# Optimization experiments

Measured on AMD Instinct MI355X. Metric: run time of the kernel, lower is better.

## Reference

```python
import jax, jax.numpy as jnp
import numpy as np

HIDDEN = 1024
HEADS = 16
HEAD = HIDDEN // HEADS


def _ternary_weight(key, shape):
    g = jax.random.normal(key, shape, dtype=jnp.float32)
    return jnp.where(jnp.abs(g) < 0.6, 0.0, jnp.sign(g)).astype(jnp.float32)


def setup_inputs() -> dict:
    key = jax.random.key(0)
    ks = jax.random.split(key, 10)
    x = jax.random.normal(ks[0], (2, 2048, HIDDEN), dtype=jnp.float32)
    d = {"x": x}
    names = ["q", "k", "v", "o"]
    for i, n in enumerate(names):
        d[f"w_{n}"] = _ternary_weight(ks[1 + i], (HIDDEN, HIDDEN))
        d[f"s_{n}"] = jnp.float32(0.02)  # per-layer dequant scale
        d[f"b_{n}"] = jax.random.normal(ks[5 + i], (HIDDEN,), dtype=jnp.float32) * 0.02
    return d


def _tlin(x, w, s, b):
    # dequantized ternary linear: x @ (s * w).T + b
    return jnp.einsum("bsh,oh->bso", x, w) * s + b


def reference(x, w_q, s_q, b_q, w_k, s_k, b_k, w_v, s_v, b_v, w_o, s_o, b_o):
    B, S, H = x.shape
    def split_heads(t):
        return t.reshape(B, S, HEADS, HEAD).transpose(0, 2, 1, 3)  # [B, nH, S, hd]
    q = split_heads(_tlin(x, w_q, s_q, b_q))
    k = split_heads(_tlin(x, w_k, s_k, b_k))
    v = split_heads(_tlin(x, w_v, s_v, b_v))
    scores = jnp.einsum("bhqd,bhkd->bhqk", q, k) / jnp.sqrt(jnp.float32(HEAD))
    attn = jax.nn.softmax(scores, axis=-1)
    ctx = jnp.einsum("bhqk,bhkd->bhqd", attn, v)
    ctx = ctx.transpose(0, 2, 1, 3).reshape(B, S, H)
    return _tlin(ctx, w_o, s_o, b_o)
```

## Files before the change

### kernel.cpp

```cpp
#include <hip/hip_runtime.h>
#include <hip/hip_bf16.h>

typedef unsigned short u16;
typedef __bf16 bf16x8 __attribute__((ext_vector_type(8)));
typedef __bf16 bf16x4 __attribute__((ext_vector_type(4)));
typedef float f32x4 __attribute__((ext_vector_type(4)));
typedef unsigned short u16x8 __attribute__((ext_vector_type(8)));

__device__ inline u16 f2bf(float f) {
    union { float f; unsigned u; } v; v.f = f;
    unsigned r = v.u + 0x7fffu + ((v.u >> 16) & 1u);
    return (u16)(r >> 16);
}

__global__ void convert_kernel(const float* __restrict__ x,
                               const float* __restrict__ wq, const float* __restrict__ wk,
                               const float* __restrict__ wv, const float* __restrict__ wo,
                               u16* __restrict__ dst) {
    long g = (long)blockIdx.x * blockDim.x + threadIdx.x;
    const float* src; long base;
    const long GX = 1048576, GW = 262144;
    if (g < GX)            { src = x;  base = 0; }
    else if (g < GX + GW)  { src = wq; base = GX; }
    else if (g < GX + 2*GW){ src = wk; base = GX + GW; }
    else if (g < GX + 3*GW){ src = wv; base = GX + 2*GW; }
    else                   { src = wo; base = GX + 3*GW; }
    long rel = g - base;
    float4 v = reinterpret_cast<const float4*>(src)[rel];
    ushort4 o;
    o.x = f2bf(v.x); o.y = f2bf(v.y); o.z = f2bf(v.z); o.w = f2bf(v.w);
    reinterpret_cast<ushort4*>(dst)[g] = o;
}

__global__ void __launch_bounds__(512)
qkv_gemm(const u16* __restrict__ x_bf,
         const u16* __restrict__ wq, const u16* __restrict__ wk, const u16* __restrict__ wv,
         const float* __restrict__ sq, const float* __restrict__ sk, const float* __restrict__ sv,
         const float* __restrict__ bq, const float* __restrict__ bk, const float* __restrict__ bv,
         u16* __restrict__ q_ws, u16* __restrict__ k_ws, u16* __restrict__ v_ws) {
    __shared__ __align__(16) u16 As[2][128 * 64];
    __shared__ __align__(16) u16 Bs[2][128 * 64];
    const int z = blockIdx.z;
    const u16* W   = (z == 0) ? wq : (z == 1) ? wk : wv;
    const float* sp = (z == 0) ? sq : (z == 1) ? sk : sv;
    const float* bp = (z == 0) ? bq : (z == 1) ? bk : bv;
    u16* dst = (z == 0) ? q_ws : (z == 1) ? k_ws : v_ws;
    const float extra = (z == 0) ? 0.125f * 1.44269504088896f : 1.0f;
    const int t0 = blockIdx.x * 128, n0 = blockIdx.y * 128;

    const int tid = threadIdx.x;
    const int wid = tid >> 6, lane = tid & 63, quad = lane >> 4, ln = lane & 15;
    const int wm = wid >> 2, wn = wid & 3;

    const bool stA = (wid < 4);
    const u16* gbase = stA ? x_bf : W;
    const int r0 = stA ? t0 : n0;
    const int cbase = (wid & 3) * 4;

    f32x4 acc[4][2];
#pragma unroll
    for (int im = 0; im < 4; im++)
#pragma unroll
        for (int in = 0; in < 2; in++) acc[im][in] = (f32x4){0.f, 0.f, 0.f, 0.f};

    const int sb   = cbase * 1024 + lane * 16;
    const int srow = sb >> 7;
    const int scb  = (sb & 127) ^ ((srow & 7) << 4);

#define Q_STAGE(buf, k0)                                                              \
    {                                                                                 \
        const u16* g = gbase + (long)(r0 + srow) * 1024 + (k0) + (scb >> 1);          \
        u16* d = (stA ? &As[buf][0] : &Bs[buf][0]) + cbase * 512;                     \
        _Pragma("unroll")                                                             \
        for (int i = 0; i < 4; i++) {                                                 \
            __builtin_amdgcn_global_load_lds(                                         \
                (const __attribute__((address_space(1))) void*)(g + (long)i * 8 * 1024), \
                (__attribute__((address_space(3))) void*)(d + i * 512), 16, 0, 0);    \
        }                                                                             \
    }

    Q_STAGE(0, 0);
    __syncthreads();

    int cur = 0;
    for (int k0 = 0; k0 < 1024; k0 += 64) {
        if (k0 + 64 < 1024) Q_STAGE(cur ^ 1, k0 + 64);
        const char* Ac = (const char*)&As[cur][0];
        const char* Bc = (const char*)&Bs[cur][0];
#pragma unroll
        for (int ks = 0; ks < 2; ks++) {
            bf16x8 af[4], bfr[2];
#pragma unroll
            for (int im = 0; im < 4; im++) {
                int r = wm * 64 + im * 16 + ln;
                int byt = (r * 128 + ks * 64 + quad * 16) ^ ((r & 7) << 4);
                af[im] = *reinterpret_cast<const bf16x8*>(Ac + byt);
            }
#pragma unroll
            for (int in = 0; in < 2; in++) {
                int r = wn * 32 + in * 16 + ln;
                int byt = (r * 128 + ks * 64 + quad * 16) ^ ((r & 7) << 4);
                bfr[in] = *reinterpret_cast<const bf16x8*>(Bc + byt);
            }
#pragma unroll
            for (int im = 0; im < 4; im++)
#pragma unroll
                for (int in = 0; in < 2; in++)
                    acc[im][in] = __builtin_amdgcn_mfma_f32_16x16x32_bf16(af[im], bfr[in], acc[im][in], 0, 0, 0);
        }
        __syncthreads();
        cur ^= 1;
    }
#undef Q_STAGE

    const float s = sp[0] * extra;
#pragma unroll
    for (int in = 0; in < 2; in++) {
        int col = n0 + wn * 32 + in * 16 + ln;
        float bias = bp[col] * extra;
        int h = col >> 6, d = col & 63;
#pragma unroll
        for (int im = 0; im < 4; im++) {
            int rbase = t0 + wm * 64 + im * 16 + quad * 4;
#pragma unroll
            for (int j2 = 0; j2 < 4; j2++) {
                int t = rbase + j2;
                int b = t >> 11, ss = t & 2047;
                int bh = b * 16 + h;
                float val = acc[im][in][j2] * s + bias;
                long idx = (z < 2) ? ((long)(bh * 2048 + ss) * 64 + d)
                                   : ((long)(bh * 64 + d) * 2048 + ss);
                dst[idx] = f2bf(val);
            }
        }
    }
}

#define LDP 72

__global__ void __launch_bounds__(512)
attn_kernel(const u16* __restrict__ q_ws, const u16* __restrict__ k_ws,
            const u16* __restrict__ v_ws, u16* __restrict__ ctx) {
    __shared__ __align__(16) u16 Kb[2][4096];
    __shared__ __align__(16) u16 Vb[2][4096];
    __shared__ u16 Pt[128 * LDP];

    const int tid = threadIdx.x;
    const int wid = tid >> 6, lane = tid & 63, quad = lane >> 4, ln = lane & 15;

    const int f   = blockIdx.x + 16 * blockIdx.y;
    const int xcd = f & 7, j = f >> 3;
    const int bh  = xcd * 4 + (j >> 4);
    const int q0  = (j & 15) * 128;

    const u16* qbase = q_ws + (long)bh * 2048 * 64;
    const u16* kbase = k_ws + (long)bh * 2048 * 64;
    const u16* vbase = v_ws + (long)bh * 64 * 2048;

    const int srow = wid * 8 + (lane >> 3);
    const int sel  = 8 * ((lane & 7) ^ ((lane >> 3) & 7));
    const int xr = (ln & 7) << 4;

    bf16x8 aq[2];
#pragma unroll
    for (int ks = 0; ks < 2; ks++)
        aq[ks] = *reinterpret_cast<const bf16x8*>(
            qbase + (long)(q0 + wid * 16 + ln) * 64 + ks * 32 + quad * 8);

    bf16x8 vones;
#pragma unroll
    for (int i = 0; i < 8; i++) vones[i] = (__bf16)1.0f;

    f32x4 acc_o[4];
    f32x4 acc_l = (f32x4){0.f, 0.f, 0.f, 0.f};
#pragma unroll
    for (int dt = 0; dt < 4; dt++) acc_o[dt] = (f32x4){0.f, 0.f, 0.f, 0.f};

    const u16* kp = kbase + (long)srow * 64 + sel;
    const u16* vp = vbase + (long)srow * 2048 + sel;

    __builtin_amdgcn_global_load_lds((const __attribute__((address_space(1))) void*)kp,
                                     (__attribute__((address_space(3))) void*)(&Kb[0][wid * 512]),
                                     16, 0, 0);
    __builtin_amdgcn_global_load_lds((const __attribute__((address_space(1))) void*)vp,
                                     (__attribute__((address_space(3))) void*)(&Vb[0][wid * 512]),
                                     16, 0, 0);
    kp += 4096; vp += 64;
    __syncthreads();

    int cur = 0;
    for (int kt = 0; kt < 2048; kt += 64) {
        if (kt + 64 < 2048) {
            __builtin_amdgcn_global_load_lds((const __attribute__((address_space(1))) void*)kp,
                                             (__attribute__((address_space(3))) void*)(&Kb[cur ^ 1][wid * 512]),
                                             16, 0, 0);
            __builtin_amdgcn_global_load_lds((const __attribute__((address_space(1))) void*)vp,
                                             (__attribute__((address_space(3))) void*)(&Vb[cur ^ 1][wid * 512]),
                                             16, 0, 0);
            kp += 4096; vp += 64;
        }
        const char* Kc = (const char*)(&Kb[cur][0]);
        const char* Vc = (const char*)(&Vb[cur][0]);

#pragma unroll
        for (int k8 = 0; k8 < 4; k8++) {
            bf16x8 a0 = *reinterpret_cast<const bf16x8*>(
                Kc + (k8 * 16 + ln) * 128 + ((quad * 16) ^ xr));
            bf16x8 a1 = *reinterpret_cast<const bf16x8*>(
                Kc + (k8 * 16 + ln) * 128 + ((64 + quad * 16) ^ xr));
            f32x4 t = (f32x4){0.f, 0.f, 0.f, 0.f};
            __builtin_amdgcn_s_setprio(1);
            t = __builtin_amdgcn_mfma_f32_16x16x32_bf16(a0, aq[0], t, 0, 0, 0);
            t = __builtin_amdgcn_mfma_f32_16x16x32_bf16(a1, aq[1], t, 0, 0, 0);
            __builtin_amdgcn_s_setprio(0);
            __bf16 p0 = (__bf16)__builtin_amdgcn_exp2f(t[0]);
            __bf16 p1 = (__bf16)__builtin_amdgcn_exp2f(t[1]);
            __bf16 p2 = (__bf16)__builtin_amdgcn_exp2f(t[2]);
            __bf16 p3 = (__bf16)__builtin_amdgcn_exp2f(t[3]);
            *reinterpret_cast<bf16x4*>(Pt + (wid * 16 + ln) * LDP + k8 * 16 + quad * 4)
                = (bf16x4){p0, p1, p2, p3};
        }

#pragma unroll
        for (int step = 0; step < 2; step++) {
            bf16x8 ap = *reinterpret_cast<const bf16x8*>(
                Pt + (wid * 16 + ln) * LDP + step * 32 + quad * 8);
            bf16x8 bv0 = *reinterpret_cast<const bf16x8*>(
                Vc + (0 * 16 + ln) * 128 + ((step * 64 + quad * 16) ^ xr));
            bf16x8 bv1 = *reinterpret_cast<const bf16x8*>(
                Vc + (1 * 16 + ln) * 128 + ((step * 64 + quad * 16) ^ xr));
            bf16x8 bv2 = *reinterpret_cast<const bf16x8*>(
                Vc + (2 * 16 + ln) * 128 + ((step * 64 + quad * 16) ^ xr));
            bf16x8 bv3 = *reinterpret_cast<const bf16x8*>(
                Vc + (3 * 16 + ln) * 128 + ((step * 64 + quad * 16) ^ xr));
            __builtin_amdgcn_s_setprio(1);
            acc_o[0] = __builtin_amdgcn_mfma_f32_16x16x32_bf16(ap, bv0, acc_o[0], 0, 0, 0);
            acc_o[1] = __builtin_amdgcn_mfma_f32_16x16x32_bf16(ap, bv1, acc_o[1], 0, 0, 0);
            acc_o[2] = __builtin_amdgcn_mfma_f32_16x16x32_bf16(ap, bv2, acc_o[2], 0, 0, 0);
            acc_o[3] = __builtin_amdgcn_mfma_f32_16x16x32_bf16(ap, bv3, acc_o[3], 0, 0, 0);
            acc_l    = __builtin_amdgcn_mfma_f32_16x16x32_bf16(ap, vones, acc_l, 0, 0, 0);
            __builtin_amdgcn_s_setprio(0);
        }
        __syncthreads();
        cur ^= 1;
    }

    const int b = bh >> 4, h = bh & 15;
#pragma unroll
    for (int j2 = 0; j2 < 4; j2++) {
        float rinv = 1.0f / acc_l[j2];
        int t = b * 2048 + q0 + wid * 16 + quad * 4 + j2;
#pragma unroll
        for (int dt = 0; dt < 4; dt++) {
            float val = acc_o[dt][j2] * rinv;
            ctx[(long)t * 1024 + h * 64 + dt * 16 + ln] = f2bf(val);
        }
    }
}

__global__ void __launch_bounds__(512)
o_gemm(const u16* __restrict__ ctx, const u16* __restrict__ wo,
       const float* __restrict__ so, const float* __restrict__ bo,
       float* __restrict__ out) {
    __shared__ __align__(16) u16 As[2][128 * 64];
    __shared__ __align__(16) u16 Bs[2][128 * 64];
    const int tid = threadIdx.x;
    const int wid = tid >> 6, lane = tid & 63, quad = lane >> 4, ln = lane & 15;
    const int wm = wid >> 2, wn = wid & 3;
    const int t0 = blockIdx.x * 128, n0 = blockIdx.y * 128;

    const bool stA = (wid < 4);
    const u16* gbase = stA ? ctx : wo;
    const int r0 = stA ? t0 : n0;
    const int cbase = (wid & 3) * 4;

    f32x4 acc[4][2];
#pragma unroll
    for (int im = 0; im < 4; im++)
#pragma unroll
        for (int in = 0; in < 2; in++) acc[im][in] = (f32x4){0.f, 0.f, 0.f, 0.f};

    const int sb   = cbase * 1024 + lane * 16;
    const int srow = sb >> 7;
    const int scb  = (sb & 127) ^ ((srow & 7) << 4);

#define O_STAGE(buf, k0)                                                              \
    {                                                                                 \
        const u16* g = gbase + (long)(r0 + srow) * 1024 + (k0) + (scb >> 1);          \
        u16* d = (stA ? &As[buf][0] : &Bs[buf][0]) + cbase * 512;                     \
        _Pragma("unroll")                                                             \
        for (int i = 0; i < 4; i++) {                                                 \
            __builtin_amdgcn_global_load_lds(                                         \
                (const __attribute__((address_space(1))) void*)(g + (long)i * 8 * 1024), \
                (__attribute__((address_space(3))) void*)(d + i * 512), 16, 0, 0);    \
        }                                                                             \
    }

    O_STAGE(0, 0);
    __syncthreads();

    int cur = 0;
    for (int k0 = 0; k0 < 1024; k0 += 64) {
        if (k0 + 64 < 1024) O_STAGE(cur ^ 1, k0 + 64);
        const char* Ac = (const char*)&As[cur][0];
        const char* Bc = (const char*)&Bs[cur][0];
#pragma unroll
        for (int ks = 0; ks < 2; ks++) {
            bf16x8 af[4], bfr[2];
#pragma unroll
            for (int im = 0; im < 4; im++) {
                int r = wm * 64 + im * 16 + ln;
                int byt = (r * 128 + ks * 64 + quad * 16) ^ ((r & 7) << 4);
                af[im] = *reinterpret_cast<const bf16x8*>(Ac + byt);
            }
#pragma unroll
            for (int in = 0; in < 2; in++) {
                int r = wn * 32 + in * 16 + ln;
                int byt = (r * 128 + ks * 64 + quad * 16) ^ ((r & 7) << 4);
                bfr[in] = *reinterpret_cast<const bf16x8*>(Bc + byt);
            }
#pragma unroll
            for (int im = 0; im < 4; im++)
#pragma unroll
                for (int in = 0; in < 2; in++)
                    acc[im][in] = __builtin_amdgcn_mfma_f32_16x16x32_bf16(af[im], bfr[in], acc[im][in], 0, 0, 0);
        }
        __syncthreads();
        cur ^= 1;
    }
#undef O_STAGE

    const float s = so[0];
#pragma unroll
    for (int in = 0; in < 2; in++) {
        int col = n0 + wn * 32 + in * 16 + ln;
        float bias = bo[col];
#pragma unroll
        for (int im = 0; im < 4; im++) {
            int rbase = t0 + wm * 64 + im * 16 + quad * 4;
#pragma unroll
            for (int j2 = 0; j2 < 4; j2++)
                out[(long)(rbase + j2) * 1024 + col] = acc[im][in][j2] * s + bias;
        }
    }
}

extern "C" void kernel_launch(void* const* d_in, const int* in_sizes, int n_in,
                              void* d_out, int out_size, void* d_ws, size_t ws_size,
                              hipStream_t stream) {
    const float* x   = (const float*)d_in[0];
    const float* w_q = (const float*)d_in[1];
    const float* s_q = (const float*)d_in[2];
    const float* b_q = (const float*)d_in[3];
    const float* w_k = (const float*)d_in[4];
    const float* s_k = (const float*)d_in[5];
    const float* b_k = (const float*)d_in[6];
    const float* w_v = (const float*)d_in[7];
    const float* s_v = (const float*)d_in[8];
    const float* b_v = (const float*)d_in[9];
    const float* w_o = (const float*)d_in[10];
    const float* s_o = (const float*)d_in[11];
    const float* b_o = (const float*)d_in[12];

    if (ws_size < (size_t)50331648) return;

    u16* ws     = (u16*)d_ws;
    u16* x_bf   = ws;
    u16* wq_bf  = x_bf  + 4194304;
    u16* wk_bf  = wq_bf + 1048576;
    u16* wv_bf  = wk_bf + 1048576;
    u16* wo_bf  = wv_bf + 1048576;
    u16* q_ws   = wo_bf + 1048576;
    u16* k_ws   = q_ws  + 4194304;
    u16* v_ws   = k_ws  + 4194304;
    u16* ctx_ws = v_ws  + 4194304;

    convert_kernel<<<dim3(8192), dim3(256), 0, stream>>>(x, w_q, w_k, w_v, w_o, ws);
    qkv_gemm<<<dim3(32, 8, 3), dim3(512), 0, stream>>>(x_bf, wq_bf, wk_bf, wv_bf,
                                                       s_q, s_k, s_v, b_q, b_k, b_v,
                                                       q_ws, k_ws, v_ws);
    attn_kernel<<<dim3(16, 32), dim3(512), 0, stream>>>(q_ws, k_ws, v_ws, ctx_ws);
    o_gemm<<<dim3(32, 8), dim3(512), 0, stream>>>(ctx_ws, wo_bf, s_o, b_o, (float*)d_out);
}
```

Measured before the change: 188.0 us.

## Process two query tiles per warp in attention to reuse K/V loads

Each attention block now covers 256 query rows instead of 128, with every warp handling two 16-row query tiles. The K and V fragments read from shared memory, and the K/V tiles staged from global memory, are reused across both query tiles, which halves the global K/V traffic per query. The cost is half as many blocks (256 instead of 512), so fewer waves are available to hide latency on a chip with 256 CUs, and each thread holds more registers and the P scratch buffer doubles.

Measured after the change: 190.5 us. Within noise of the previous version (+1.3%).

```diff
diff --git a/kernel.cpp b/kernel.cpp
--- a/kernel.cpp
+++ b/kernel.cpp
@@ -143,15 +143,15 @@
             const u16* __restrict__ v_ws, u16* __restrict__ ctx) {
     __shared__ __align__(16) u16 Kb[2][4096];
     __shared__ __align__(16) u16 Vb[2][4096];
-    __shared__ u16 Pt[128 * LDP];
+    __shared__ u16 Pt[256 * LDP];
 
     const int tid = threadIdx.x;
     const int wid = tid >> 6, lane = tid & 63, quad = lane >> 4, ln = lane & 15;
 
-    const int f   = blockIdx.x + 16 * blockIdx.y;
+    const int f   = blockIdx.x + 8 * blockIdx.y;
     const int xcd = f & 7, j = f >> 3;
-    const int bh  = xcd * 4 + (j >> 4);
-    const int q0  = (j & 15) * 128;
+    const int bh  = xcd * 4 + (j >> 3);
+    const int q0  = (j & 7) * 256;
 
     const u16* qbase = q_ws + (long)bh * 2048 * 64;
     const u16* kbase = k_ws + (long)bh * 2048 * 64;
@@ -161,20 +161,26 @@
     const int sel  = 8 * ((lane & 7) ^ ((lane >> 3) & 7));
     const int xr = (ln & 7) << 4;
 
-    bf16x8 aq[2];
-#pragma unroll
-    for (int ks = 0; ks < 2; ks++)
-        aq[ks] = *reinterpret_cast<const bf16x8*>(
-            qbase + (long)(q0 + wid * 16 + ln) * 64 + ks * 32 + quad * 8);
+    bf16x8 aq[2][2];
+#pragma unroll
+    for (int qt = 0; qt < 2; qt++)
+#pragma unroll
+        for (int ks = 0; ks < 2; ks++)
+            aq[qt][ks] = *reinterpret_cast<const bf16x8*>(
+                qbase + (long)(q0 + wid * 32 + qt * 16 + ln) * 64 + ks * 32 + quad * 8);
 
     bf16x8 vones;
 #pragma unroll
     for (int i = 0; i < 8; i++) vones[i] = (__bf16)1.0f;
 
-    f32x4 acc_o[4];
-    f32x4 acc_l = (f32x4){0.f, 0.f, 0.f, 0.f};
-#pragma unroll
-    for (int dt = 0; dt < 4; dt++) acc_o[dt] = (f32x4){0.f, 0.f, 0.f, 0.f};
+    f32x4 acc_o[2][4];
+    f32x4 acc_l[2];
+#pragma unroll
+    for (int qt = 0; qt < 2; qt++) {
+        acc_l[qt] = (f32x4){0.f, 0.f, 0.f, 0.f};
+#pragma unroll
+        for (int dt = 0; dt < 4; dt++) acc_o[qt][dt] = (f32x4){0.f, 0.f, 0.f, 0.f};
+    }
 
     const u16* kp = kbase + (long)srow * 64 + sel;
     const u16* vp = vbase + (long)srow * 2048 + sel;
@@ -208,23 +214,29 @@
                 Kc + (k8 * 16 + ln) * 128 + ((quad * 16) ^ xr));
             bf16x8 a1 = *reinterpret_cast<const bf16x8*>(
                 Kc + (k8 * 16 + ln) * 128 + ((64 + quad * 16) ^ xr));
-            f32x4 t = (f32x4){0.f, 0.f, 0.f, 0.f};
-            __builtin_amdgcn_s_setprio(1);
-            t = __builtin_amdgcn_mfma_f32_16x16x32_bf16(a0, aq[0], t, 0, 0, 0);
-            t = __builtin_amdgcn_mfma_f32_16x16x32_bf16(a1, aq[1], t, 0, 0, 0);
-            __builtin_amdgcn_s_setprio(0);
-            __bf16 p0 = (__bf16)__builtin_amdgcn_exp2f(t[0]);
-            __bf16 p1 = (__bf16)__builtin_amdgcn_exp2f(t[1]);
-            __bf16 p2 = (__bf16)__builtin_amdgcn_exp2f(t[2]);
-            __bf16 p3 = (__bf16)__builtin_amdgcn_exp2f(t[3]);
-            *reinterpret_cast<bf16x4*>(Pt + (wid * 16 + ln) * LDP + k8 * 16 + quad * 4)
-                = (bf16x4){p0, p1, p2, p3};
+#pragma unroll
+            for (int qt = 0; qt < 2; qt++) {
+                f32x4 t = (f32x4){0.f, 0.f, 0.f, 0.f};
+                __builtin_amdgcn_s_setprio(1);
+                t = __builtin_amdgcn_mfma_f32_16x16x32_bf16(a0, aq[qt][0], t, 0, 0, 0);
+                t = __builtin_amdgcn_mfma_f32_16x16x32_bf16(a1, aq[qt][1], t, 0, 0, 0);
+                __builtin_amdgcn_s_setprio(0);
+                __bf16 p0 = (__bf16)__builtin_amdgcn_exp2f(t[0]);
+                __bf16 p1 = (__bf16)__builtin_amdgcn_exp2f(t[1]);
+                __bf16 p2 = (__bf16)__builtin_amdgcn_exp2f(t[2]);
+                __bf16 p3 = (__bf16)__builtin_amdgcn_exp2f(t[3]);
+                *reinterpret_cast<bf16x4*>(
+                    Pt + (wid * 32 + qt * 16 + ln) * LDP + k8 * 16 + quad * 4)
+                    = (bf16x4){p0, p1, p2, p3};
+            }
         }
 
 #pragma unroll
         for (int step = 0; step < 2; step++) {
-            bf16x8 ap = *reinterpret_cast<const bf16x8*>(
-                Pt + (wid * 16 + ln) * LDP + step * 32 + quad * 8);
+            bf16x8 ap0 = *reinterpret_cast<const bf16x8*>(
+                Pt + (wid * 32 + ln) * LDP + step * 32 + quad * 8);
+            bf16x8 ap1 = *reinterpret_cast<const bf16x8*>(
+                Pt + (wid * 32 + 16 + ln) * LDP + step * 32 + quad * 8);
             bf16x8 bv0 = *reinterpret_cast<const bf16x8*>(
                 Vc + (0 * 16 + ln) * 128 + ((step * 64 + quad * 16) ^ xr));
             bf16x8 bv1 = *reinterpret_cast<const bf16x8*>(
@@ -234,11 +246,16 @@
             bf16x8 bv3 = *reinterpret_cast<const bf16x8*>(
                 Vc + (3 * 16 + ln) * 128 + ((step * 64 + quad * 16) ^ xr));
             __builtin_amdgcn_s_setprio(1);
-            acc_o[0] = __builtin_amdgcn_mfma_f32_16x16x32_bf16(ap, bv0, acc_o[0], 0, 0, 0);
-            acc_o[1] = __builtin_amdgcn_mfma_f32_16x16x32_bf16(ap, bv1, acc_o[1], 0, 0, 0);
-            acc_o[2] = __builtin_amdgcn_mfma_f32_16x16x32_bf16(ap, bv2, acc_o[2], 0, 0, 0);
-            acc_o[3] = __builtin_amdgcn_mfma_f32_16x16x32_bf16(ap, bv3, acc_o[3], 0, 0, 0);
-            acc_l    = __builtin_amdgcn_mfma_f32_16x16x32_bf16(ap, vones, acc_l, 0, 0, 0);
+            acc_o[0][0] = __builtin_amdgcn_mfma_f32_16x16x32_bf16(ap0, bv0, acc_o[0][0], 0, 0, 0);
+            acc_o[0][1] = __builtin_amdgcn_mfma_f32_16x16x32_bf16(ap0, bv1, acc_o[0][1], 0, 0, 0);
+            acc_o[0][2] = __builtin_amdgcn_mfma_f32_16x16x32_bf16(ap0, bv2, acc_o[0][2], 0, 0, 0);
+            acc_o[0][3] = __builtin_amdgcn_mfma_f32_16x16x32_bf16(ap0, bv3, acc_o[0][3], 0, 0, 0);
+            acc_l[0]    = __builtin_amdgcn_mfma_f32_16x16x32_bf16(ap0, vones, acc_l[0], 0, 0, 0);
+            acc_o[1][0] = __builtin_amdgcn_mfma_f32_16x16x32_bf16(ap1, bv0, acc_o[1][0], 0, 0, 0);
+            acc_o[1][1] = __builtin_amdgcn_mfma_f32_16x16x32_bf16(ap1, bv1, acc_o[1][1], 0, 0, 0);
+            acc_o[1][2] = __builtin_amdgcn_mfma_f32_16x16x32_bf16(ap1, bv2, acc_o[1][2], 0, 0, 0);
+            acc_o[1][3] = __builtin_amdgcn_mfma_f32_16x16x32_bf16(ap1, bv3, acc_o[1][3], 0, 0, 0);
+            acc_l[1]    = __builtin_amdgcn_mfma_f32_16x16x32_bf16(ap1, vones, acc_l[1], 0, 0, 0);
             __builtin_amdgcn_s_setprio(0);
         }
         __syncthreads();
@@ -247,13 +264,16 @@
 
     const int b = bh >> 4, h = bh & 15;
 #pragma unroll
-    for (int j2 = 0; j2 < 4; j2++) {
-        float rinv = 1.0f / acc_l[j2];
-        int t = b * 2048 + q0 + wid * 16 + quad * 4 + j2;
-#pragma unroll
-        for (int dt = 0; dt < 4; dt++) {
-            float val = acc_o[dt][j2] * rinv;
-            ctx[(long)t * 1024 + h * 64 + dt * 16 + ln] = f2bf(val);
+    for (int qt = 0; qt < 2; qt++) {
+#pragma unroll
+        for (int j2 = 0; j2 < 4; j2++) {
+            float rinv = 1.0f / acc_l[qt][j2];
+            int t = b * 2048 + q0 + wid * 32 + qt * 16 + quad * 4 + j2;
+#pragma unroll
+            for (int dt = 0; dt < 4; dt++) {
+                float val = acc_o[qt][dt][j2] * rinv;
+                ctx[(long)t * 1024 + h * 64 + dt * 16 + ln] = f2bf(val);
+            }
         }
     }
 }
@@ -379,6 +399,6 @@
     qkv_gemm<<<dim3(32, 8, 3), dim3(512), 0, stream>>>(x_bf, wq_bf, wk_bf, wv_bf,
                                                        s_q, s_k, s_v, b_q, b_k, b_v,
                                                        q_ws, k_ws, v_ws);
-    attn_kernel<<<dim3(16, 32), dim3(512), 0, stream>>>(q_ws, k_ws, v_ws, ctx_ws);
+    attn_kernel<<<dim3(8, 32), dim3(512), 0, stream>>>(q_ws, k_ws, v_ws, ctx_ws);
     o_gemm<<<dim3(32, 8), dim3(512), 0, stream>>>(ctx_ws, wo_bf, s_o, b_o, (float*)d_out);
 }
```

## Fuse Q/K/V projections into one GEMM block sharing the x tile

Applied to the files above, without the earlier changes.

The QKV GEMM drops the z-dimension grid split. Each block now loads one x tile and the three matching weight tiles, and accumulates Q, K and V outputs together, so x is read from global memory and staged into LDS once instead of three times. MFMA sections are also wrapped in s_setprio raises. In exchange the block count falls from 768 to 256, LDS use roughly doubles (about 128KB), and the accumulator register count triples, which can reduce occupancy and parallelism across the CUs.

Result: no change. 185.5 us (median of 2 runs) (-1.3%).

```diff
diff --git a/kernel.cpp b/kernel.cpp
--- a/kernel.cpp
+++ b/kernel.cpp
@@ -38,99 +38,115 @@
          const float* __restrict__ sq, const float* __restrict__ sk, const float* __restrict__ sv,
          const float* __restrict__ bq, const float* __restrict__ bk, const float* __restrict__ bv,
          u16* __restrict__ q_ws, u16* __restrict__ k_ws, u16* __restrict__ v_ws) {
-    __shared__ __align__(16) u16 As[2][128 * 64];
-    __shared__ __align__(16) u16 Bs[2][128 * 64];
-    const int z = blockIdx.z;
-    const u16* W   = (z == 0) ? wq : (z == 1) ? wk : wv;
-    const float* sp = (z == 0) ? sq : (z == 1) ? sk : sv;
-    const float* bp = (z == 0) ? bq : (z == 1) ? bk : bv;
-    u16* dst = (z == 0) ? q_ws : (z == 1) ? k_ws : v_ws;
-    const float extra = (z == 0) ? 0.125f * 1.44269504088896f : 1.0f;
+    __shared__ __align__(16) u16 As[2][8192];
+    __shared__ __align__(16) u16 Bs[2][3 * 8192];
     const int t0 = blockIdx.x * 128, n0 = blockIdx.y * 128;
 
     const int tid = threadIdx.x;
     const int wid = tid >> 6, lane = tid & 63, quad = lane >> 4, ln = lane & 15;
     const int wm = wid >> 2, wn = wid & 3;
 
-    const bool stA = (wid < 4);
-    const u16* gbase = stA ? x_bf : W;
+    const bool stA = (wid < 2);
+    const int zz = stA ? 0 : ((wid - 2) >> 1);
+    const u16* Wz = (zz == 0) ? wq : (zz == 1) ? wk : wv;
+    const u16* gbase = stA ? x_bf : Wz;
     const int r0 = stA ? t0 : n0;
-    const int cbase = (wid & 3) * 4;
-
-    f32x4 acc[4][2];
-#pragma unroll
-    for (int im = 0; im < 4; im++)
-#pragma unroll
-        for (int in = 0; in < 2; in++) acc[im][in] = (f32x4){0.f, 0.f, 0.f, 0.f};
-
-    const int sb   = cbase * 1024 + lane * 16;
-    const int srow = sb >> 7;
-    const int scb  = (sb & 127) ^ ((srow & 7) << 4);
-
-#define Q_STAGE(buf, k0)                                                              \
+    const int ccb = stA ? (wid * 8) : (((wid - 2) & 1) * 8);
+
+    const int lrow = lane >> 3;
+    const int sel  = 8 * ((lane & 7) ^ lrow);
+
+    f32x4 acc[3][4][2];
+#pragma unroll
+    for (int z = 0; z < 3; z++)
+#pragma unroll
+        for (int im = 0; im < 4; im++)
+#pragma unroll
+            for (int in = 0; in < 2; in++) acc[z][im][in] = (f32x4){0.f, 0.f, 0.f, 0.f};
+
+#define QK_STAGE(buf, k0)                                                             \
     {                                                                                 \
-        const u16* g = gbase + (long)(r0 + srow) * 1024 + (k0) + (scb >> 1);          \
-        u16* d = (stA ? &As[buf][0] : &Bs[buf][0]) + cbase * 512;                     \
+        u16* dbase = stA ? &As[buf][0] : &Bs[buf][zz * 8192];                         \
         _Pragma("unroll")                                                             \
-        for (int i = 0; i < 4; i++) {                                                 \
+        for (int i = 0; i < 8; i++) {                                                 \
+            int cc = ccb + i;                                                         \
+            const u16* g = gbase + (long)(r0 + cc * 8 + lrow) * 1024 + (k0) + sel;    \
             __builtin_amdgcn_global_load_lds(                                         \
-                (const __attribute__((address_space(1))) void*)(g + (long)i * 8 * 1024), \
-                (__attribute__((address_space(3))) void*)(d + i * 512), 16, 0, 0);    \
+                (const __attribute__((address_space(1))) void*)g,                     \
+                (__attribute__((address_space(3))) void*)(dbase + cc * 512), 16, 0, 0); \
         }                                                                             \
     }
 
-    Q_STAGE(0, 0);
+    QK_STAGE(0, 0);
     __syncthreads();
 
     int cur = 0;
     for (int k0 = 0; k0 < 1024; k0 += 64) {
-        if (k0 + 64 < 1024) Q_STAGE(cur ^ 1, k0 + 64);
+        if (k0 + 64 < 1024) QK_STAGE(cur ^ 1, k0 + 64);
         const char* Ac = (const char*)&As[cur][0];
         const char* Bc = (const char*)&Bs[cur][0];
 #pragma unroll
         for (int ks = 0; ks < 2; ks++) {
-            bf16x8 af[4], bfr[2];
+            bf16x8 af[4];
 #pragma unroll
             for (int im = 0; im < 4; im++) {
                 int r = wm * 64 + im * 16 + ln;
                 int byt = (r * 128 + ks * 64 + quad * 16) ^ ((r & 7) << 4);
                 af[im] = *reinterpret_cast<const bf16x8*>(Ac + byt);
             }
-#pragma unroll
-            for (int in = 0; in < 2; in++) {
-                int r = wn * 32 + in * 16 + ln;
-                int byt = (r * 128 + ks * 64 + quad * 16) ^ ((r & 7) << 4);
-                bfr[in] = *reinterpret_cast<const bf16x8*>(Bc + byt);
+            int rb = wn * 32 + ln;
+#pragma unroll
+            for (int z = 0; z < 3; z++) {
+                bf16x8 b0, b1;
+                {
+                    int r = rb;
+                    int byt = (r * 128 + ks * 64 + quad * 16) ^ ((r & 7) << 4);
+                    b0 = *reinterpret_cast<const bf16x8*>(Bc + z * 16384 + byt);
+                    r = rb + 16;
+                    byt = (r * 128 + ks * 64 + quad * 16) ^ ((r & 7) << 4);
+                    b1 = *reinterpret_cast<const bf16x8*>(Bc + z * 16384 + byt);
+                }
+                __builtin_amdgcn_s_setprio(1);
+#pragma unroll
+                for (int im = 0; im < 4; im++) {
+                    acc[z][im][0] = __builtin_amdgcn_mfma_f32_16x16x32_bf16(af[im], b0, acc[z][im][0], 0, 0, 0);
+                    acc[z][im][1] = __builtin_amdgcn_mfma_f32_16x16x32_bf16(af[im], b1, acc[z][im][1], 0, 0, 0);
+                }
+                __builtin_amdgcn_s_setprio(0);
             }
-#pragma unroll
-            for (int im = 0; im < 4; im++)
-#pragma unroll
-                for (int in = 0; in < 2; in++)
-                    acc[im][in] = __builtin_amdgcn_mfma_f32_16x16x32_bf16(af[im], bfr[in], acc[im][in], 0, 0, 0);
         }
         __syncthreads();
         cur ^= 1;
     }
-#undef Q_STAGE
-
-    const float s = sp[0] * extra;
-#pragma unroll
-    for (int in = 0; in < 2; in++) {
-        int col = n0 + wn * 32 + in * 16 + ln;
-        float bias = bp[col] * extra;
-        int h = col >> 6, d = col & 63;
-#pragma unroll
-        for (int im = 0; im < 4; im++) {
-            int rbase = t0 + wm * 64 + im * 16 + quad * 4;
-#pragma unroll
-            for (int j2 = 0; j2 < 4; j2++) {
-                int t = rbase + j2;
-                int b = t >> 11, ss = t & 2047;
-                int bh = b * 16 + h;
-                float val = acc[im][in][j2] * s + bias;
-                long idx = (z < 2) ? ((long)(bh * 2048 + ss) * 64 + d)
-                                   : ((long)(bh * 64 + d) * 2048 + ss);
-                dst[idx] = f2bf(val);
+#undef QK_STAGE
+
+    const float sq_ = sq[0] * 0.125f * 1.44269504088896f;
+    const float sk_ = sk[0];
+    const float sv_ = sv[0];
+#pragma unroll
+    for (int z = 0; z < 3; z++) {
+        u16* dst = (z == 0) ? q_ws : (z == 1) ? k_ws : v_ws;
+        const float* bp = (z == 0) ? bq : (z == 1) ? bk : bv;
+        const float s = (z == 0) ? sq_ : (z == 1) ? sk_ : sv_;
+        const float be = (z == 0) ? 0.125f * 1.44269504088896f : 1.0f;
+#pragma unroll
+        for (int in = 0; in < 2; in++) {
+            int col = n0 + wn * 32 + in * 16 + ln;
+            float bias = bp[col] * be;
+            int h = col >> 6, d = col & 63;
+#pragma unroll
+            for (int im = 0; im < 4; im++) {
+                int rbase = t0 + wm * 64 + im * 16 + quad * 4;
+#pragma unroll
+                for (int j2 = 0; j2 < 4; j2++) {
+                    int t = rbase + j2;
+                    int b = t >> 11, ss = t & 2047;
+                    int bh = b * 16 + h;
+                    float val = acc[z][im][in][j2] * s + bias;
+                    long idx = (z < 2) ? ((long)(bh * 2048 + ss) * 64 + d)
+                                       : ((long)(bh * 64 + d) * 2048 + ss);
+                    dst[idx] = f2bf(val);
+                }
             }
         }
     }
@@ -376,9 +392,9 @@
     u16* ctx_ws = v_ws  + 4194304;
 
     convert_kernel<<<dim3(8192), dim3(256), 0, stream>>>(x, w_q, w_k, w_v, w_o, ws);
-    qkv_gemm<<<dim3(32, 8, 3), dim3(512), 0, stream>>>(x_bf, wq_bf, wk_bf, wv_bf,
-                                                       s_q, s_k, s_v, b_q, b_k, b_v,
-                                                       q_ws, k_ws, v_ws);
+    qkv_gemm<<<dim3(32, 8), dim3(512), 0, stream>>>(x_bf, wq_bf, wk_bf, wv_bf,
+                                                    s_q, s_k, s_v, b_q, b_k, b_v,
+                                                    q_ws, k_ws, v_ws);
     attn_kernel<<<dim3(16, 32), dim3(512), 0, stream>>>(q_ws, k_ws, v_ws, ctx_ws);
     o_gemm<<<dim3(32, 8), dim3(512), 0, stream>>>(ctx_ws, wo_bf, s_o, b_o, (float*)d_out);
 }
```
